# Kernel optimization log

Measured on AMD Instinct MI355X. Metric: run time of the kernel, lower is better.

## Reference

```python
import jax, jax.numpy as jnp
import numpy as np

BLOCK = 16
NUM_HEADS = 12
EMBED = 768
LN_EPS = 1e-6


def setup_inputs() -> dict:
    key = jax.random.key(0)
    ks = jax.random.split(key, 6)
    H = W = 1024
    x = jax.random.normal(ks[0], (H, W), dtype=jnp.float32)
    # Conv2d(1, EMBED, kernel=BLOCK, stride=BLOCK) weights, flattened to [E, b*b]
    proj_w = jax.random.normal(ks[1], (EMBED, BLOCK * BLOCK), dtype=jnp.float32) * 0.02
    proj_b = jax.random.normal(ks[2], (EMBED,), dtype=jnp.float32) * 0.02
    ln_g = jnp.ones((EMBED,), dtype=jnp.float32)
    ln_b = jnp.zeros((EMBED,), dtype=jnp.float32)
    # nn.Linear(E, 3E, bias=False): weight [3E, E]
    qkv_w = jax.random.normal(ks[3], (3 * EMBED, EMBED), dtype=jnp.float32) * 0.02
    return {"x": x, "proj_w": proj_w, "proj_b": proj_b,
            "ln_g": ln_g, "ln_b": ln_b, "qkv_w": qkv_w}


def reference(x, proj_w, proj_b, ln_g, ln_b, qkv_w):
    H, W = x.shape
    b = BLOCK
    # Patch embed: conv with kernel=stride=b on a single-channel image is
    # exactly patchify + matmul. Token order matches flatten(2) (row-major).
    patches = x.reshape(H // b, b, W // b, b).transpose(0, 2, 1, 3)
    patches = patches.reshape((H // b) * (W // b), b * b)      # [N, b*b]
    tok = patches @ proj_w.T + proj_b                          # [N, E]

    # LayerNorm (eps=1e-6)
    mu = jnp.mean(tok, axis=-1, keepdims=True)
    var = jnp.mean(jnp.square(tok - mu), axis=-1, keepdims=True)
    tok = (tok - mu) * jax.lax.rsqrt(var + LN_EPS) * ln_g + ln_b

    # Attention (batch = 1)
    N, C = tok.shape
    h, d = NUM_HEADS, C // NUM_HEADS
    qkv = (tok @ qkv_w.T).reshape(N, 3, h, d)                  # [N, 3, h, d]
    q = qkv[:, 0].transpose(1, 0, 2)                            # [h, N, d]
    k = qkv[:, 1].transpose(1, 0, 2)
    v = qkv[:, 2].transpose(1, 0, 2)
    scale = d ** -0.5
    attn = jax.nn.softmax(jnp.einsum('hnd,hmd->hnm', q, k) * scale, axis=-1)
    out = jnp.einsum('hnm,hmd->hnd', attn, v)                   # [h, N, d]
    out = out.transpose(1, 0, 2).reshape(N, C)                  # [N, C]
    return out[None]                                            # [1, N, C]
```

## Files before the change

kernel.cpp:

```cpp
#include <hip/hip_runtime.h>
#include <hip/hip_bf16.h>

typedef __bf16 bf16_t;
typedef __attribute__((ext_vector_type(8))) __bf16 bf16x8;
typedef __attribute__((ext_vector_type(4))) __bf16 bf16x4;
typedef __attribute__((ext_vector_type(4))) float f32x4;
typedef __attribute__((ext_vector_type(4))) unsigned int uint4v;

#define QSCALE 0.1803368801111204f

static __device__ inline void glds16(const bf16_t* g, bf16_t* l) {
    __builtin_amdgcn_global_load_lds(
        (__attribute__((address_space(1))) const void*)g,
        (__attribute__((address_space(3))) void*)l,
        16, 0, 0);
}

static __device__ inline float hwexp2(float x) {
#if __has_builtin(__builtin_amdgcn_exp2f)
    return __builtin_amdgcn_exp2f(x);
#else
    float r;
    asm("v_exp_f32 %0, %1" : "=v"(r) : "v"(x));
    return r;
#endif
}

static __device__ inline unsigned int pack_trunc(float lo, float hi) {
    return __builtin_amdgcn_perm(__builtin_bit_cast(unsigned int, hi),
                                 __builtin_bit_cast(unsigned int, lo),
                                 0x07060302u);
}

__global__ void cvt_kernel(const float* __restrict__ in, bf16_t* __restrict__ out, int n4) {
    int i = blockIdx.x * 256 + threadIdx.x;
    if (i < n4) {
        float4 v = ((const float4*)in)[i];
        bf16x4 o = {(bf16_t)v.x, (bf16_t)v.y, (bf16_t)v.z, (bf16_t)v.w};
        ((bf16x4*)out)[i] = o;
    }
}

__global__ __launch_bounds__(256) void patch_gemm(const float* __restrict__ x,
                                                  const float* __restrict__ pw,
                                                  const float* __restrict__ pb,
                                                  float* __restrict__ tok) {
    const int bn = blockIdx.x;
    const int bm = blockIdx.y;
    const int tid = threadIdx.x;

    __shared__ bf16_t At[64][264];
    __shared__ bf16_t Bt[64][264];

    #pragma unroll
    for (int t = 0; t < 16; t++) {
        int linear = tid + t * 256;
        int ml = linear >> 6;
        int kv = (linear & 63) << 2;
        int n = bm * 64 + ml;
        int pr = n >> 6, pc = n & 63;
        int i = kv >> 4, j = kv & 15;
        float4 v = *(const float4*)(x + (pr * 16 + i) * 1024 + pc * 16 + j);
        bf16x4 o = {(bf16_t)v.x, (bf16_t)v.y, (bf16_t)v.z, (bf16_t)v.w};
        *(bf16x4*)(&At[ml][kv]) = o;
    }
    #pragma unroll
    for (int t = 0; t < 8; t++) {
        int linear = tid + t * 256;
        int nl = linear >> 5;
        int kv = (linear & 31) << 3;
        const float* src = pw + (size_t)(bn * 64 + nl) * 256 + kv;
        float4 v0 = *(const float4*)(src);
        float4 v1 = *(const float4*)(src + 4);
        bf16x8 o = {(bf16_t)v0.x, (bf16_t)v0.y, (bf16_t)v0.z, (bf16_t)v0.w,
                    (bf16_t)v1.x, (bf16_t)v1.y, (bf16_t)v1.z, (bf16_t)v1.w};
        *(bf16x8*)(&Bt[nl][kv]) = o;
    }
    __syncthreads();

    const int lane = tid & 63, wid = tid >> 6, ln = lane & 15, quad = lane >> 4;
    f32x4 acc[4];
    #pragma unroll
    for (int s = 0; s < 4; s++) acc[s] = {0.f, 0.f, 0.f, 0.f};

    #pragma unroll
    for (int kk = 0; kk < 8; kk++) {
        bf16x8 af = *(const bf16x8*)(&At[wid * 16 + ln][kk * 32 + quad * 8]);
        #pragma unroll
        for (int s = 0; s < 4; s++) {
            bf16x8 bfr = *(const bf16x8*)(&Bt[s * 16 + ln][kk * 32 + quad * 8]);
            acc[s] = __builtin_amdgcn_mfma_f32_16x16x32_bf16(af, bfr, acc[s], 0, 0, 0);
        }
    }

    #pragma unroll
    for (int s = 0; s < 4; s++) {
        int e = bn * 64 + s * 16 + ln;
        float bias = pb[e];
        #pragma unroll
        for (int r = 0; r < 4; r++) {
            int m = bm * 64 + wid * 16 + quad * 4 + r;
            tok[(size_t)m * 768 + e] = acc[s][r] + bias;
        }
    }
}

__global__ __launch_bounds__(256) void ln_kernel(const float* __restrict__ tok,
                                                 const float* __restrict__ g,
                                                 const float* __restrict__ b,
                                                 bf16_t* __restrict__ out) {
    const int n = blockIdx.x;
    const int tid = threadIdx.x;
    const float* row = tok + (size_t)n * 768;
    float x0 = row[tid], x1 = row[tid + 256], x2 = row[tid + 512];
    float s = x0 + x1 + x2;
    float s2 = x0 * x0 + x1 * x1 + x2 * x2;
    #pragma unroll
    for (int off = 32; off; off >>= 1) {
        s += __shfl_xor(s, off);
        s2 += __shfl_xor(s2, off);
    }
    __shared__ float ws1[4], ws2[4];
    int wid = tid >> 6;
    if ((tid & 63) == 0) { ws1[wid] = s; ws2[wid] = s2; }
    __syncthreads();
    s = ws1[0] + ws1[1] + ws1[2] + ws1[3];
    s2 = ws2[0] + ws2[1] + ws2[2] + ws2[3];
    float mu = s * (1.f / 768.f);
    float var = s2 * (1.f / 768.f) - mu * mu;
    float r = rsqrtf(var + 1e-6f);
    bf16_t* orow = out + (size_t)n * 768;
    orow[tid]       = (bf16_t)((x0 - mu) * r * g[tid]       + b[tid]);
    orow[tid + 256] = (bf16_t)((x1 - mu) * r * g[tid + 256] + b[tid + 256]);
    orow[tid + 512] = (bf16_t)((x2 - mu) * r * g[tid + 512] + b[tid + 512]);
}

__global__ __launch_bounds__(256) void qkv_gemm(const bf16_t* __restrict__ tokb,
                                                const bf16_t* __restrict__ wq,
                                                bf16_t* __restrict__ qb,
                                                bf16_t* __restrict__ kswz,
                                                bf16_t* __restrict__ vswz) {
    const int bn = blockIdx.x;
    const int bm = blockIdx.y;
    const int tid = threadIdx.x;
    const int wid = tid >> 6, lane = tid & 63;
    const int ln = lane & 15, quad = lane >> 4;
    const int wm = wid & 1, wn = wid >> 1;

    __shared__ bf16_t Asw[2][8192];
    __shared__ bf16_t Bsw[2][4096];

    f32x4 acc[4][2];
    #pragma unroll
    for (int sm = 0; sm < 4; sm++)
        #pragma unroll
        for (int sn = 0; sn < 2; sn++) acc[sm][sn] = {0.f, 0.f, 0.f, 0.f};

    auto stage = [&](int kb0, int buf) {
        #pragma unroll
        for (int i = 0; i < 4; i++) {
            int L = wid * 256 + i * 64 + lane;
            int r = L >> 3, c = L & 7;
            int gc = c ^ (r & 7);
            glds16(tokb + (size_t)(bm * 128 + r) * 768 + kb0 + gc * 8,
                   Asw[buf] + (wid * 256 + i * 64) * 8);
        }
        #pragma unroll
        for (int i = 0; i < 2; i++) {
            int L = wid * 128 + i * 64 + lane;
            int r = L >> 3, c = L & 7;
            int gc = c ^ (r & 7);
            glds16(wq + (size_t)(bn * 64 + r) * 768 + kb0 + gc * 8,
                   Bsw[buf] + (wid * 128 + i * 64) * 8);
        }
    };

    auto compute = [&](const bf16_t* Ab, const bf16_t* Bb) {
        #pragma unroll
        for (int kk = 0; kk < 2; kk++) {
            const int c = (kk * 4 + quad) ^ (ln & 7);
            bf16x8 af[4], bfr[2];
            #pragma unroll
            for (int sm = 0; sm < 4; sm++) {
                int row = wm * 64 + sm * 16 + ln;
                af[sm] = *(const bf16x8*)(Ab + (row * 8 + c) * 8);
            }
            #pragma unroll
            for (int sn = 0; sn < 2; sn++) {
                int row = wn * 32 + sn * 16 + ln;
                bfr[sn] = *(const bf16x8*)(Bb + (row * 8 + c) * 8);
            }
            #pragma unroll
            for (int sm = 0; sm < 4; sm++)
                #pragma unroll
                for (int sn = 0; sn < 2; sn++)
                    acc[sm][sn] = __builtin_amdgcn_mfma_f32_16x16x32_bf16(af[sm], bfr[sn], acc[sm][sn], 0, 0, 0);
        }
    };

    stage(0, 0);

    for (int s = 0; s < 12; s += 2) {
        __builtin_amdgcn_s_barrier();
        stage((s + 1) * 64, 1);
        __builtin_amdgcn_s_waitcnt(0x0F76);
        __builtin_amdgcn_s_barrier();
        compute(Asw[0], Bsw[0]);
        __builtin_amdgcn_s_barrier();
        if (s + 2 < 12) {
            stage((s + 2) * 64, 0);
            __builtin_amdgcn_s_waitcnt(0x0F76);
        } else {
            __builtin_amdgcn_s_waitcnt(0x0F70);
        }
        __builtin_amdgcn_s_barrier();
        compute(Asw[1], Bsw[1]);
    }

    const int sidx = bn / 12;
    const int head = bn % 12;
    #pragma unroll
    for (int sn = 0; sn < 2; sn++) {
        int dc = wn * 32 + sn * 16 + ln;
        #pragma unroll
        for (int sm = 0; sm < 4; sm++) {
            #pragma unroll
            for (int r = 0; r < 4; r++) {
                int m = bm * 128 + wm * 64 + sm * 16 + quad * 4 + r;
                float v = acc[sm][sn][r];
                if (sidx == 0) {
                    qb[((size_t)(head * 4096 + m)) * 64 + dc] = (bf16_t)(v * QSCALE);
                } else if (sidx == 1) {
                    bf16_t val = (bf16_t)v;
                    int kt = m >> 6, sb = (m >> 4) & 3, lnk = m & 15;
                    int half = dc >> 5, quadk = (dc >> 3) & 3, j = dc & 7;
                    int l = quadk * 16 + lnk;
                    kswz[((size_t)(head * 64 + kt)) * 4096 + sb * 1024 + half * 512 + l * 8 + j] = val;
                } else {
                    bf16_t val = (bf16_t)v;
                    int kt = m >> 6, keyl = m & 63;
                    int sblk = keyl >> 4;
                    int mm = sblk >> 1, tb = sblk & 1;
                    int w16 = keyl & 15, qv = w16 >> 2, jj = w16 & 3;
                    int jp = tb * 4 + jj;
                    int db = dc >> 4, lnv = dc & 15;
                    int l = qv * 16 + lnv;
                    vswz[((size_t)(head * 64 + kt)) * 4096 + ((mm * 4 + db) * 64 + l) * 8 + jp] = val;
                }
            }
        }
    }
}

__global__ __launch_bounds__(256, 2) void attn_partial(const bf16_t* __restrict__ qbuf,
                                                       const bf16_t* __restrict__ kswz,
                                                       const bf16_t* __restrict__ vswz,
                                                       float* __restrict__ raw0,
                                                       float* __restrict__ raw1,
                                                       float* __restrict__ l_part) {
    const int h = blockIdx.y;
    const int chunk = blockIdx.z;
    const int tid = threadIdx.x;
    const int wid = tid >> 6;
    const int lane = tid & 63;
    const int ln = lane & 15, quad = lane >> 4;
    const int qh = wid & 1;
    const int kh = wid >> 1;
    const int q0 = blockIdx.x * 128;

    __shared__ bf16_t SMEM[2][2][2][4096];

    bf16x8 qf[4][2];
    #pragma unroll
    for (int g = 0; g < 4; g++) {
        const int q0g = q0 + qh * 64 + g * 16;
        const bf16_t* qrow = qbuf + ((size_t)h * 4096 + q0g + ln) * 64;
        qf[g][0] = *(const bf16x8*)(qrow + quad * 8);
        qf[g][1] = *(const bf16x8*)(qrow + 32 + quad * 8);
    }

    bf16x8 ones;
    #pragma unroll
    for (int i = 0; i < 8; i++) ones[i] = (bf16_t)1.0f;

    const bf16_t* kg = kswz + (size_t)h * 64 * 4096 + (size_t)(chunk * 32 + kh * 16) * 4096;
    const bf16_t* vg = vswz + (size_t)h * 64 * 4096 + (size_t)(chunk * 32 + kh * 16) * 4096;

    f32x4 accO[4][4];
    f32x4 accL[4];
    #pragma unroll
    for (int g = 0; g < 4; g++) {
        accL[g] = {0.f, 0.f, 0.f, 0.f};
        #pragma unroll
        for (int d = 0; d < 4; d++) accO[g][d] = {0.f, 0.f, 0.f, 0.f};
    }

    auto stage = [&](int tile, int buf) {
        const bf16_t* kt_g = kg + (size_t)tile * 4096;
        const bf16_t* vt_g = vg + (size_t)tile * 4096;
        bf16_t* kl = &SMEM[0][kh][buf][qh * 2048];
        bf16_t* vl = &SMEM[1][kh][buf][qh * 2048];
        #pragma unroll
        for (int i = 0; i < 4; i++) {
            glds16(kt_g + qh * 2048 + i * 512 + lane * 8, kl + i * 512);
            glds16(vt_g + qh * 2048 + i * 512 + lane * 8, vl + i * 512);
        }
    };

    auto compute = [&](const bf16_t* Kb, const bf16_t* Vb) {
        #pragma unroll
        for (int m = 0; m < 2; m++) {
            bf16x8 vf[4];
            #pragma unroll
            for (int db = 0; db < 4; db++)
                vf[db] = *(const bf16x8*)(Vb + m * 2048 + db * 512 + lane * 8);
            bf16x8 kfa0 = *(const bf16x8*)(Kb + (2 * m) * 1024 + lane * 8);
            bf16x8 kfa1 = *(const bf16x8*)(Kb + (2 * m) * 1024 + 512 + lane * 8);
            bf16x8 kfb0 = *(const bf16x8*)(Kb + (2 * m + 1) * 1024 + lane * 8);
            bf16x8 kfb1 = *(const bf16x8*)(Kb + (2 * m + 1) * 1024 + 512 + lane * 8);
            #pragma unroll
            for (int g = 0; g < 4; g++) {
                f32x4 z = {0.f, 0.f, 0.f, 0.f};
                f32x4 SA = __builtin_amdgcn_mfma_f32_16x16x32_bf16(kfa0, qf[g][0], z, 0, 0, 0);
                SA = __builtin_amdgcn_mfma_f32_16x16x32_bf16(kfa1, qf[g][1], SA, 0, 0, 0);
                f32x4 SB = __builtin_amdgcn_mfma_f32_16x16x32_bf16(kfb0, qf[g][0], z, 0, 0, 0);
                SB = __builtin_amdgcn_mfma_f32_16x16x32_bf16(kfb1, qf[g][1], SB, 0, 0, 0);

                float e0 = hwexp2(SA[0]), e1 = hwexp2(SA[1]), e2 = hwexp2(SA[2]), e3 = hwexp2(SA[3]);
                float e4 = hwexp2(SB[0]), e5 = hwexp2(SB[1]), e6 = hwexp2(SB[2]), e7 = hwexp2(SB[3]);
                uint4v u = {pack_trunc(e0, e1), pack_trunc(e2, e3),
                            pack_trunc(e4, e5), pack_trunc(e6, e7)};
                bf16x8 pb = __builtin_bit_cast(bf16x8, u);
                accL[g] = __builtin_amdgcn_mfma_f32_16x16x32_bf16(ones, pb, accL[g], 0, 0, 0);
                #pragma unroll
                for (int db = 0; db < 4; db++)
                    accO[g][db] = __builtin_amdgcn_mfma_f32_16x16x32_bf16(vf[db], pb, accO[g][db], 0, 0, 0);
            }
        }
    };

    stage(0, 0);

    for (int kt = 0; kt < 16; kt += 2) {
        __builtin_amdgcn_s_barrier();
        stage(kt + 1, 1);
        __builtin_amdgcn_s_waitcnt(0x0F78);
        __builtin_amdgcn_s_barrier();
        compute(&SMEM[0][kh][0][0], &SMEM[1][kh][0][0]);
        __builtin_amdgcn_s_barrier();
        if (kt + 2 < 16) {
            stage(kt + 2, 0);
            __builtin_amdgcn_s_waitcnt(0x0F78);
        } else {
            __builtin_amdgcn_s_waitcnt(0x0F70);
        }
        __builtin_amdgcn_s_barrier();
        compute(&SMEM[0][kh][1][0], &SMEM[1][kh][1][0]);
    }

    __syncthreads();
    float* comb  = (float*)&SMEM[0][0][0][0];
    float* combl = (float*)((char*)&SMEM[0][0][0][0] + 36864);
    if (kh == 1) {
        #pragma unroll
        for (int g = 0; g < 4; g++) {
            const int lq = qh * 64 + g * 16 + ln;
            #pragma unroll
            for (int db = 0; db < 4; db++)
                *(f32x4*)&comb[lq * 68 + db * 16 + quad * 4] = accO[g][db];
            if (quad == 0) combl[lq] = accL[g][0];
        }
    }
    __syncthreads();
    if (kh == 0) {
        float* base = chunk ? raw1 : raw0;
        #pragma unroll
        for (int g = 0; g < 4; g++) {
            const int lq = qh * 64 + g * 16 + ln;
            const int qg = q0 + lq;
            float lsum = accL[g][0] + combl[lq];
            if (quad == 0) l_part[(size_t)chunk * 49152 + h * 4096 + qg] = lsum;
            float* op = base + (size_t)qg * 768 + h * 64 + quad * 4;
            #pragma unroll
            for (int db = 0; db < 4; db++) {
                f32x4 o = accO[g][db] + *(const f32x4*)&comb[lq * 68 + db * 16 + quad * 4];
                *(f32x4*)(op + db * 16) = o;
            }
        }
    }
}

__global__ __launch_bounds__(256) void norm_kernel(const float* __restrict__ raw0,
                                                   const float* __restrict__ raw1,
                                                   const float* __restrict__ l_part,
                                                   float* __restrict__ out) {
    const int q = blockIdx.x;
    const int tid = threadIdx.x;
    __shared__ float linv[12];
    if (tid < 12)
        linv[tid] = 1.0f / (l_part[tid * 4096 + q] + l_part[49152 + tid * 4096 + q]);
    __syncthreads();
    #pragma unroll
    for (int t = 0; t < 3; t++) {
        int c = tid + t * 256;
        size_t idx = (size_t)q * 768 + c;
        out[idx] = (raw0[idx] + raw1[idx]) * linv[c >> 6];
    }
}

extern "C" void kernel_launch(void* const* d_in, const int* in_sizes, int n_in,
                              void* d_out, int out_size, void* d_ws, size_t ws_size,
                              hipStream_t stream) {
    const float* x      = (const float*)d_in[0];
    const float* proj_w = (const float*)d_in[1];
    const float* proj_b = (const float*)d_in[2];
    const float* ln_g   = (const float*)d_in[3];
    const float* ln_b   = (const float*)d_in[4];
    const float* qkv_w  = (const float*)d_in[5];
    float* out = (float*)d_out;

    char* ws = (char*)d_ws;
    float*  tok_pre = (float*)(ws + 0);
    bf16_t* tok_b   = (bf16_t*)(ws + 12582912);
    bf16_t* pw_b    = (bf16_t*)(ws + 18874368);
    bf16_t* qw_b    = (bf16_t*)(ws + 19267584);
    bf16_t* qbuf    = (bf16_t*)(ws + 22806528);
    bf16_t* kswz    = (bf16_t*)(ws + 29097984);
    bf16_t* vswz    = (bf16_t*)(ws + 35389440);
    float*  raw0    = tok_pre;
    float*  raw1    = out;
    float*  l_part  = (float*)pw_b;

    cvt_kernel<<<1728, 256, 0, stream>>>(qkv_w, qw_b, 442368);
    patch_gemm<<<dim3(12, 64), 256, 0, stream>>>(x, proj_w, proj_b, tok_pre);
    ln_kernel<<<4096, 256, 0, stream>>>(tok_pre, ln_g, ln_b, tok_b);
    qkv_gemm<<<dim3(36, 32), 256, 0, stream>>>(tok_b, qw_b, qbuf, kswz, vswz);
    attn_partial<<<dim3(32, 12, 2), 256, 0, stream>>>(qbuf, kswz, vswz, raw0, raw1, l_part);
    norm_kernel<<<4096, 256, 0, stream>>>(raw0, raw1, l_part, out);
}
```

Measured before the change: 176.2 us.

## Halve attention K/V staging tiles to fit three blocks per CU

```diff
diff --git a/kernel.cpp b/kernel.cpp
--- a/kernel.cpp
+++ b/kernel.cpp
@@ -252,7 +252,7 @@
     }
 }
 
-__global__ __launch_bounds__(256, 2) void attn_partial(const bf16_t* __restrict__ qbuf,
+__global__ __launch_bounds__(256, 3) void attn_partial(const bf16_t* __restrict__ qbuf,
                                                        const bf16_t* __restrict__ kswz,
                                                        const bf16_t* __restrict__ vswz,
                                                        float* __restrict__ raw0,
@@ -268,7 +268,9 @@
     const int kh = wid >> 1;
     const int q0 = blockIdx.x * 128;
 
-    __shared__ bf16_t SMEM[2][2][2][4096];
+    __shared__ __align__(16) char RAW[35328];
+    bf16_t* Kst = (bf16_t*)RAW;
+    bf16_t* Vst = (bf16_t*)(RAW + 16384);
 
     bf16x8 qf[4][2];
     #pragma unroll
@@ -295,72 +297,74 @@
         for (int d = 0; d < 4; d++) accO[g][d] = {0.f, 0.f, 0.f, 0.f};
     }
 
-    auto stage = [&](int tile, int buf) {
-        const bf16_t* kt_g = kg + (size_t)tile * 4096;
-        const bf16_t* vt_g = vg + (size_t)tile * 4096;
-        bf16_t* kl = &SMEM[0][kh][buf][qh * 2048];
-        bf16_t* vl = &SMEM[1][kh][buf][qh * 2048];
-        #pragma unroll
-        for (int i = 0; i < 4; i++) {
-            glds16(kt_g + qh * 2048 + i * 512 + lane * 8, kl + i * 512);
-            glds16(vt_g + qh * 2048 + i * 512 + lane * 8, vl + i * 512);
+    auto stage = [&](int ht, int buf) {
+        const bf16_t* kt_g = kg + (size_t)ht * 2048;
+        const bf16_t* vt_g = vg + (size_t)ht * 2048;
+        bf16_t* kl = Kst + (kh * 2 + buf) * 2048 + qh * 1024;
+        bf16_t* vl = Vst + (kh * 2 + buf) * 2048 + qh * 1024;
+        #pragma unroll
+        for (int i = 0; i < 2; i++) {
+            glds16(kt_g + qh * 1024 + i * 512 + lane * 8, kl + i * 512);
+            glds16(vt_g + qh * 1024 + i * 512 + lane * 8, vl + i * 512);
         }
     };
 
     auto compute = [&](const bf16_t* Kb, const bf16_t* Vb) {
-        #pragma unroll
-        for (int m = 0; m < 2; m++) {
-            bf16x8 vf[4];
+        bf16x8 vf[4];
+        #pragma unroll
+        for (int db = 0; db < 4; db++)
+            vf[db] = *(const bf16x8*)(Vb + db * 512 + lane * 8);
+        bf16x8 kfa0 = *(const bf16x8*)(Kb + lane * 8);
+        bf16x8 kfa1 = *(const bf16x8*)(Kb + 512 + lane * 8);
+        bf16x8 kfb0 = *(const bf16x8*)(Kb + 1024 + lane * 8);
+        bf16x8 kfb1 = *(const bf16x8*)(Kb + 1536 + lane * 8);
+        #pragma unroll
+        for (int g = 0; g < 4; g++) {
+            f32x4 z = {0.f, 0.f, 0.f, 0.f};
+            f32x4 SA = __builtin_amdgcn_mfma_f32_16x16x32_bf16(kfa0, qf[g][0], z, 0, 0, 0);
+            SA = __builtin_amdgcn_mfma_f32_16x16x32_bf16(kfa1, qf[g][1], SA, 0, 0, 0);
+            f32x4 SB = __builtin_amdgcn_mfma_f32_16x16x32_bf16(kfb0, qf[g][0], z, 0, 0, 0);
+            SB = __builtin_amdgcn_mfma_f32_16x16x32_bf16(kfb1, qf[g][1], SB, 0, 0, 0);
+
+            float e0 = hwexp2(SA[0]), e1 = hwexp2(SA[1]), e2 = hwexp2(SA[2]), e3 = hwexp2(SA[3]);
+            float e4 = hwexp2(SB[0]), e5 = hwexp2(SB[1]), e6 = hwexp2(SB[2]), e7 = hwexp2(SB[3]);
+            uint4v u = {pack_trunc(e0, e1), pack_trunc(e2, e3),
+                        pack_trunc(e4, e5), pack_trunc(e6, e7)};
+            bf16x8 pb = __builtin_bit_cast(bf16x8, u);
+            accL[g] = __builtin_amdgcn_mfma_f32_16x16x32_bf16(ones, pb, accL[g], 0, 0, 0);
             #pragma unroll
             for (int db = 0; db < 4; db++)
-                vf[db] = *(const bf16x8*)(Vb + m * 2048 + db * 512 + lane * 8);
-            bf16x8 kfa0 = *(const bf16x8*)(Kb + (2 * m) * 1024 + lane * 8);
-            bf16x8 kfa1 = *(const bf16x8*)(Kb + (2 * m) * 1024 + 512 + lane * 8);
-            bf16x8 kfb0 = *(const bf16x8*)(Kb + (2 * m + 1) * 1024 + lane * 8);
-            bf16x8 kfb1 = *(const bf16x8*)(Kb + (2 * m + 1) * 1024 + 512 + lane * 8);
-            #pragma unroll
-            for (int g = 0; g < 4; g++) {
-                f32x4 z = {0.f, 0.f, 0.f, 0.f};
-                f32x4 SA = __builtin_amdgcn_mfma_f32_16x16x32_bf16(kfa0, qf[g][0], z, 0, 0, 0);
-                SA = __builtin_amdgcn_mfma_f32_16x16x32_bf16(kfa1, qf[g][1], SA, 0, 0, 0);
-                f32x4 SB = __builtin_amdgcn_mfma_f32_16x16x32_bf16(kfb0, qf[g][0], z, 0, 0, 0);
-                SB = __builtin_amdgcn_mfma_f32_16x16x32_bf16(kfb1, qf[g][1], SB, 0, 0, 0);
-
-                float e0 = hwexp2(SA[0]), e1 = hwexp2(SA[1]), e2 = hwexp2(SA[2]), e3 = hwexp2(SA[3]);
-                float e4 = hwexp2(SB[0]), e5 = hwexp2(SB[1]), e6 = hwexp2(SB[2]), e7 = hwexp2(SB[3]);
-                uint4v u = {pack_trunc(e0, e1), pack_trunc(e2, e3),
-                            pack_trunc(e4, e5), pack_trunc(e6, e7)};
-                bf16x8 pb = __builtin_bit_cast(bf16x8, u);
-                accL[g] = __builtin_amdgcn_mfma_f32_16x16x32_bf16(ones, pb, accL[g], 0, 0, 0);
-                #pragma unroll
-                for (int db = 0; db < 4; db++)
-                    accO[g][db] = __builtin_amdgcn_mfma_f32_16x16x32_bf16(vf[db], pb, accO[g][db], 0, 0, 0);
-            }
+                accO[g][db] = __builtin_amdgcn_mfma_f32_16x16x32_bf16(vf[db], pb, accO[g][db], 0, 0, 0);
         }
     };
 
     stage(0, 0);
 
-    for (int kt = 0; kt < 16; kt += 2) {
-        __builtin_amdgcn_s_barrier();
-        stage(kt + 1, 1);
-        __builtin_amdgcn_s_waitcnt(0x0F78);
-        __builtin_amdgcn_s_barrier();
-        compute(&SMEM[0][kh][0][0], &SMEM[1][kh][0][0]);
-        __builtin_amdgcn_s_barrier();
-        if (kt + 2 < 16) {
-            stage(kt + 2, 0);
-            __builtin_amdgcn_s_waitcnt(0x0F78);
+    const bf16_t* K0 = Kst + (kh * 2 + 0) * 2048;
+    const bf16_t* V0 = Vst + (kh * 2 + 0) * 2048;
+    const bf16_t* K1 = Kst + (kh * 2 + 1) * 2048;
+    const bf16_t* V1 = Vst + (kh * 2 + 1) * 2048;
+
+    for (int ht = 0; ht < 32; ht += 2) {
+        __builtin_amdgcn_s_barrier();
+        stage(ht + 1, 1);
+        __builtin_amdgcn_s_waitcnt(0x0F74);
+        __builtin_amdgcn_s_barrier();
+        compute(K0, V0);
+        __builtin_amdgcn_s_barrier();
+        if (ht + 2 < 32) {
+            stage(ht + 2, 0);
+            __builtin_amdgcn_s_waitcnt(0x0F74);
         } else {
             __builtin_amdgcn_s_waitcnt(0x0F70);
         }
         __builtin_amdgcn_s_barrier();
-        compute(&SMEM[0][kh][1][0], &SMEM[1][kh][1][0]);
+        compute(K1, V1);
     }
 
     __syncthreads();
-    float* comb  = (float*)&SMEM[0][0][0][0];
-    float* combl = (float*)((char*)&SMEM[0][0][0][0] + 36864);
+    float* comb  = (float*)RAW;
+    float* combl = (float*)(RAW + 34816);
     if (kh == 1) {
         #pragma unroll
         for (int g = 0; g < 4; g++) {
```

Measured after the change: 253.2 us. 1.44x slower.

## Load K/V fragments directly to registers and compute row sums with VALU

Applied to the files above, without the earlier changes.

```diff
diff --git a/kernel.cpp b/kernel.cpp
--- a/kernel.cpp
+++ b/kernel.cpp
@@ -30,6 +30,10 @@
     return __builtin_amdgcn_perm(__builtin_bit_cast(unsigned int, hi),
                                  __builtin_bit_cast(unsigned int, lo),
                                  0x07060302u);
+}
+
+static __device__ inline float btrunc(float x) {
+    return __builtin_bit_cast(float, __builtin_bit_cast(unsigned int, x) & 0xFFFF0000u);
 }
 
 __global__ void cvt_kernel(const float* __restrict__ in, bf16_t* __restrict__ out, int n4) {
@@ -268,7 +272,7 @@
     const int kh = wid >> 1;
     const int q0 = blockIdx.x * 128;
 
-    __shared__ bf16_t SMEM[2][2][2][4096];
+    __shared__ __align__(16) float COMB[128 * 68 + 128];
 
     bf16x8 qf[4][2];
     #pragma unroll
@@ -279,88 +283,68 @@
         qf[g][1] = *(const bf16x8*)(qrow + 32 + quad * 8);
     }
 
-    bf16x8 ones;
-    #pragma unroll
-    for (int i = 0; i < 8; i++) ones[i] = (bf16_t)1.0f;
-
     const bf16_t* kg = kswz + (size_t)h * 64 * 4096 + (size_t)(chunk * 32 + kh * 16) * 4096;
     const bf16_t* vg = vswz + (size_t)h * 64 * 4096 + (size_t)(chunk * 32 + kh * 16) * 4096;
 
     f32x4 accO[4][4];
-    f32x4 accL[4];
+    float lsum[4];
     #pragma unroll
     for (int g = 0; g < 4; g++) {
-        accL[g] = {0.f, 0.f, 0.f, 0.f};
+        lsum[g] = 0.f;
         #pragma unroll
         for (int d = 0; d < 4; d++) accO[g][d] = {0.f, 0.f, 0.f, 0.f};
     }
 
-    auto stage = [&](int tile, int buf) {
-        const bf16_t* kt_g = kg + (size_t)tile * 4096;
-        const bf16_t* vt_g = vg + (size_t)tile * 4096;
-        bf16_t* kl = &SMEM[0][kh][buf][qh * 2048];
-        bf16_t* vl = &SMEM[1][kh][buf][qh * 2048];
+    auto loadF = [&](int ht, bf16x8* kf, bf16x8* vf) {
+        const bf16_t* kp = kg + (size_t)ht * 2048 + lane * 8;
+        const bf16_t* vp = vg + (size_t)ht * 2048 + lane * 8;
         #pragma unroll
         for (int i = 0; i < 4; i++) {
-            glds16(kt_g + qh * 2048 + i * 512 + lane * 8, kl + i * 512);
-            glds16(vt_g + qh * 2048 + i * 512 + lane * 8, vl + i * 512);
+            kf[i] = *(const bf16x8*)(kp + i * 512);
+            vf[i] = *(const bf16x8*)(vp + i * 512);
         }
     };
 
-    auto compute = [&](const bf16_t* Kb, const bf16_t* Vb) {
-        #pragma unroll
-        for (int m = 0; m < 2; m++) {
-            bf16x8 vf[4];
+    auto computeF = [&](const bf16x8* kf, const bf16x8* vf) {
+        #pragma unroll
+        for (int g = 0; g < 4; g++) {
+            f32x4 z = {0.f, 0.f, 0.f, 0.f};
+            f32x4 SA = __builtin_amdgcn_mfma_f32_16x16x32_bf16(kf[0], qf[g][0], z, 0, 0, 0);
+            SA = __builtin_amdgcn_mfma_f32_16x16x32_bf16(kf[1], qf[g][1], SA, 0, 0, 0);
+            f32x4 SB = __builtin_amdgcn_mfma_f32_16x16x32_bf16(kf[2], qf[g][0], z, 0, 0, 0);
+            SB = __builtin_amdgcn_mfma_f32_16x16x32_bf16(kf[3], qf[g][1], SB, 0, 0, 0);
+
+            float e0 = hwexp2(SA[0]), e1 = hwexp2(SA[1]), e2 = hwexp2(SA[2]), e3 = hwexp2(SA[3]);
+            float e4 = hwexp2(SB[0]), e5 = hwexp2(SB[1]), e6 = hwexp2(SB[2]), e7 = hwexp2(SB[3]);
+            lsum[g] += ((btrunc(e0) + btrunc(e1)) + (btrunc(e2) + btrunc(e3)))
+                     + ((btrunc(e4) + btrunc(e5)) + (btrunc(e6) + btrunc(e7)));
+            uint4v u = {pack_trunc(e0, e1), pack_trunc(e2, e3),
+                        pack_trunc(e4, e5), pack_trunc(e6, e7)};
+            bf16x8 pb = __builtin_bit_cast(bf16x8, u);
             #pragma unroll
             for (int db = 0; db < 4; db++)
-                vf[db] = *(const bf16x8*)(Vb + m * 2048 + db * 512 + lane * 8);
-            bf16x8 kfa0 = *(const bf16x8*)(Kb + (2 * m) * 1024 + lane * 8);
-            bf16x8 kfa1 = *(const bf16x8*)(Kb + (2 * m) * 1024 + 512 + lane * 8);
-            bf16x8 kfb0 = *(const bf16x8*)(Kb + (2 * m + 1) * 1024 + lane * 8);
-            bf16x8 kfb1 = *(const bf16x8*)(Kb + (2 * m + 1) * 1024 + 512 + lane * 8);
-            #pragma unroll
-            for (int g = 0; g < 4; g++) {
-                f32x4 z = {0.f, 0.f, 0.f, 0.f};
-                f32x4 SA = __builtin_amdgcn_mfma_f32_16x16x32_bf16(kfa0, qf[g][0], z, 0, 0, 0);
-                SA = __builtin_amdgcn_mfma_f32_16x16x32_bf16(kfa1, qf[g][1], SA, 0, 0, 0);
-                f32x4 SB = __builtin_amdgcn_mfma_f32_16x16x32_bf16(kfb0, qf[g][0], z, 0, 0, 0);
-                SB = __builtin_amdgcn_mfma_f32_16x16x32_bf16(kfb1, qf[g][1], SB, 0, 0, 0);
-
-                float e0 = hwexp2(SA[0]), e1 = hwexp2(SA[1]), e2 = hwexp2(SA[2]), e3 = hwexp2(SA[3]);
-                float e4 = hwexp2(SB[0]), e5 = hwexp2(SB[1]), e6 = hwexp2(SB[2]), e7 = hwexp2(SB[3]);
-                uint4v u = {pack_trunc(e0, e1), pack_trunc(e2, e3),
-                            pack_trunc(e4, e5), pack_trunc(e6, e7)};
-                bf16x8 pb = __builtin_bit_cast(bf16x8, u);
-                accL[g] = __builtin_amdgcn_mfma_f32_16x16x32_bf16(ones, pb, accL[g], 0, 0, 0);
-                #pragma unroll
-                for (int db = 0; db < 4; db++)
-                    accO[g][db] = __builtin_amdgcn_mfma_f32_16x16x32_bf16(vf[db], pb, accO[g][db], 0, 0, 0);
-            }
+                accO[g][db] = __builtin_amdgcn_mfma_f32_16x16x32_bf16(vf[db], pb, accO[g][db], 0, 0, 0);
         }
     };
 
-    stage(0, 0);
-
-    for (int kt = 0; kt < 16; kt += 2) {
-        __builtin_amdgcn_s_barrier();
-        stage(kt + 1, 1);
-        __builtin_amdgcn_s_waitcnt(0x0F78);
-        __builtin_amdgcn_s_barrier();
-        compute(&SMEM[0][kh][0][0], &SMEM[1][kh][0][0]);
-        __builtin_amdgcn_s_barrier();
-        if (kt + 2 < 16) {
-            stage(kt + 2, 0);
-            __builtin_amdgcn_s_waitcnt(0x0F78);
-        } else {
-            __builtin_amdgcn_s_waitcnt(0x0F70);
-        }
-        __builtin_amdgcn_s_barrier();
-        compute(&SMEM[0][kh][1][0], &SMEM[1][kh][1][0]);
-    }
-
-    __syncthreads();
-    float* comb  = (float*)&SMEM[0][0][0][0];
-    float* combl = (float*)((char*)&SMEM[0][0][0][0] + 36864);
+    bf16x8 kA[4], vA[4], kB[4], vB[4];
+    loadF(0, kA, vA);
+
+    for (int ht = 0; ht < 32; ht += 2) {
+        loadF(ht + 1, kB, vB);
+        computeF(kA, vA);
+        if (ht + 2 < 32) loadF(ht + 2, kA, vA);
+        computeF(kB, vB);
+    }
+
+    #pragma unroll
+    for (int g = 0; g < 4; g++) {
+        lsum[g] += __shfl_xor(lsum[g], 16);
+        lsum[g] += __shfl_xor(lsum[g], 32);
+    }
+
+    float* comb  = COMB;
+    float* combl = COMB + 128 * 68;
     if (kh == 1) {
         #pragma unroll
         for (int g = 0; g < 4; g++) {
@@ -368,7 +352,7 @@
             #pragma unroll
             for (int db = 0; db < 4; db++)
                 *(f32x4*)&comb[lq * 68 + db * 16 + quad * 4] = accO[g][db];
-            if (quad == 0) combl[lq] = accL[g][0];
+            if (quad == 0) combl[lq] = lsum[g];
         }
     }
     __syncthreads();
@@ -378,8 +362,8 @@
         for (int g = 0; g < 4; g++) {
             const int lq = qh * 64 + g * 16 + ln;
             const int qg = q0 + lq;
-            float lsum = accL[g][0] + combl[lq];
-            if (quad == 0) l_part[(size_t)chunk * 49152 + h * 4096 + qg] = lsum;
+            float ltot = lsum[g] + combl[lq];
+            if (quad == 0) l_part[(size_t)chunk * 49152 + h * 4096 + qg] = ltot;
             float* op = base + (size_t)qg * 768 + h * 64 + quad * 4;
             #pragma unroll
             for (int db = 0; db < 4; db++) {
```

Result: slower. 179.9 us (+2.1%).
